# Kernel tuning notes

Measured on AMD Instinct MI355X. Metric: run time of the kernel, lower is better.

The kernel has to match this reference:

```python
import jax, jax.numpy as jnp
import numpy as np

N_USERS = 100000
N_ITEMS = 50000
N_NODES = N_USERS + N_ITEMS
LATENT = 64
NNZ = 2400000
BATCH = 2048
EPS = 1e-12  # F.normalize eps


def setup_inputs() -> dict:
    key = jax.random.key(0)
    ks = jax.random.split(key, 16)
    inp = {
        "rows": jax.random.randint(ks[0], (NNZ,), 0, N_NODES, dtype=jnp.int32),
        "cols": jax.random.randint(ks[1], (NNZ,), 0, N_NODES, dtype=jnp.int32),
        "vals": jax.random.uniform(ks[2], (NNZ,), dtype=jnp.float32),
        "x": jax.random.normal(ks[3], (N_NODES, LATENT), dtype=jnp.float32) * 0.1,
        "users": jax.random.randint(ks[12], (BATCH,), 0, N_USERS, dtype=jnp.int32),
        "items": jax.random.randint(ks[13], (BATCH,), 0, N_ITEMS, dtype=jnp.int32),
    }
    for k in range(2):
        inp[f"W_gc{k}"] = jax.random.normal(ks[4 + 4 * k], (LATENT, LATENT), dtype=jnp.float32) * 0.1
        inp[f"b_gc{k}"] = jax.random.normal(ks[5 + 4 * k], (1, LATENT), dtype=jnp.float32) * 0.1
        inp[f"W_bi{k}"] = jax.random.normal(ks[6 + 4 * k], (LATENT, LATENT), dtype=jnp.float32) * 0.1
        inp[f"b_bi{k}"] = jax.random.normal(ks[7 + 4 * k], (1, LATENT), dtype=jnp.float32) * 0.1
    return inp


def _l2_normalize(v):
    # F.normalize(p=2, dim=1): divide by max(||v||_2, eps)
    n = jnp.sqrt(jnp.sum(v * v, axis=1, keepdims=True))
    return v / jnp.maximum(n, EPS)


def reference(rows, cols, vals, x,
              W_gc0, b_gc0, W_bi0, b_bi0,
              W_gc1, b_gc1, W_bi1, b_bi1,
              users, items):
    weights = [(W_gc0, b_gc0, W_bi0, b_bi0), (W_gc1, b_gc1, W_bi1, b_bi1)]
    ego = x                      # [N, D]
    embs = [x]
    for (Wg, bg, Wb, bb) in weights:
        # sparse adj @ ego  (COO gather + segment-sum scatter)
        msgs = vals[:, None] * ego[cols]                              # [nnz, D]
        side = jax.ops.segment_sum(msgs, rows, num_segments=N_NODES)  # [N, D]
        sum_emb = side @ Wg + bg
        bi_emb = (ego * side) @ Wb + bb
        ego = _l2_normalize(jax.nn.leaky_relu(sum_emb + bi_emb, negative_slope=0.2))
        embs.append(ego)
    all_emb = jnp.concatenate(embs, axis=1)          # [N, 3*D]
    users_emb = all_emb[users]                       # [B, 3*D]
    items_emb = all_emb[N_USERS + items]             # [B, 3*D]
    gamma = jnp.sum(users_emb * items_emb, axis=1)   # [B]
    return gamma
```

## Files before the change

### kernel.cpp

```cpp
#include <hip/hip_runtime.h>

#define N_USERS_C 100000
#define N_NODES_C 150000
#define D 64
#define NB 2344
#define NSUP 74
#define CPAD 16
#define SPAD 68
#define FCAP 1536
#define S1B 256
#define FRAG 240
#define S2CAP 2560
#define BPS 16
#define FPB (S1B / BPS)

__global__ __launch_bounds__(256) void mark1_k(
    const int* __restrict__ u, const int* __restrict__ it,
    unsigned char* __restrict__ samp, unsigned char* __restrict__ need, int batch)
{
    int i = blockIdx.x * blockDim.x + threadIdx.x;
    if (i >= 2 * batch) return;
    int n = (i < batch) ? u[i] : N_USERS_C + it[i - batch];
    samp[n] = 1;
    need[n] = 1;
}

__global__ __launch_bounds__(256) void mark2_k(
    const int* __restrict__ rows, const int* __restrict__ cols,
    const unsigned char* __restrict__ samp, unsigned char* __restrict__ need, int nnz)
{
    int gtid = blockIdx.x * blockDim.x + threadIdx.x;
    int stride = gridDim.x * blockDim.x;
    for (int e = gtid; e < nnz; e += stride)
        if (samp[rows[e]]) need[cols[e]] = 1;
}

__global__ __launch_bounds__(1024) void scan1_k(
    const unsigned char* __restrict__ need, int* __restrict__ part,
    int* __restrict__ bsum, int n)
{
    __shared__ int wsum[16];
    int i = blockIdx.x * 1024 + threadIdx.x;
    int lane = threadIdx.x & 63, wid = threadIdx.x >> 6;
    int v = (i < n) ? (int)need[i] : 0;
    int incl = v;
    #pragma unroll
    for (int off = 1; off < 64; off <<= 1) {
        int t = __shfl_up(incl, off);
        if (lane >= off) incl += t;
    }
    if (lane == 63) wsum[wid] = incl;
    __syncthreads();
    int woff = 0;
    for (int w = 0; w < wid; ++w) woff += wsum[w];
    if (i < n) part[i] = woff + incl - v;
    if (threadIdx.x == 1023) bsum[blockIdx.x] = woff + incl;
}

__global__ __launch_bounds__(1024) void scan2_k(
    int* __restrict__ bsum, int nb, int* __restrict__ Mptr)
{
    __shared__ int wsum[16];
    int lane = threadIdx.x & 63, wid = threadIdx.x >> 6;
    int i = threadIdx.x;
    int v = (i < nb) ? bsum[i] : 0;
    int incl = v;
    #pragma unroll
    for (int off = 1; off < 64; off <<= 1) {
        int t = __shfl_up(incl, off);
        if (lane >= off) incl += t;
    }
    if (lane == 63) wsum[wid] = incl;
    __syncthreads();
    int woff = 0;
    for (int w = 0; w < wid; ++w) woff += wsum[w];
    if (i < nb) bsum[i] = woff + incl - v;
    if (i == nb - 1) Mptr[0] = woff + incl;
}

__global__ __launch_bounds__(256) void scan3_k(
    const int* __restrict__ bsum, int* __restrict__ idx,
    const unsigned char* __restrict__ need, int* __restrict__ list, int n)
{
    int i = blockIdx.x * blockDim.x + threadIdx.x;
    if (i >= n) return;
    int t = idx[i] + bsum[i >> 10];
    if (need[i]) { idx[i] = t; list[t] = i; }
    else idx[i] = -1;
}

__global__ __launch_bounds__(256) void initcur_k(int* __restrict__ bcur)
{
    int i = blockIdx.x * blockDim.x + threadIdx.x;
    if (i < NB) bcur[i * CPAD] = i * FCAP;
}

__global__ __launch_bounds__(512) void s1_k(
    const int* __restrict__ rows, const int* __restrict__ cols,
    const float* __restrict__ vals, const int* __restrict__ idx,
    int2* __restrict__ pairs1, int* __restrict__ scnt, int nnz)
{
    __shared__ int lcur[NSUP];
    int t = threadIdx.x;
    for (int i = t; i < NSUP; i += 512) lcur[i] = 0;
    __syncthreads();
    int b = blockIdx.x;
    int per = (nnz + S1B - 1) / S1B;
    int s = b * per;
    int e = min(nnz, s + per);
    for (int i = s + t; i < e; i += 512) {
        int ci = idx[rows[i]];
        if (ci < 0) continue;
        int sp = ci >> 11;
        int k = atomicAdd(&lcur[sp], 1);
        pairs1[(size_t)sp * (S1B * FRAG) + b * FRAG + k] =
            make_int2(((ci & 2047) << 18) | cols[i], __float_as_int(vals[i]));
    }
    __syncthreads();
    for (int i = t; i < NSUP; i += 512) scnt[i * S1B + b] = lcur[i];
}

__global__ __launch_bounds__(256) void s2_k(
    const int* __restrict__ scnt, const int2* __restrict__ pairs1,
    int* __restrict__ bcurP, int2* __restrict__ pairs)
{
    __shared__ int2 sbuf[S2CAP];
    __shared__ int fcnt[32], fcur[32], gb[32];
    int sp = blockIdx.x / BPS, part = blockIdx.x % BPS;
    int t = threadIdx.x;
    if (t < 32) { fcnt[t] = 0; fcur[t] = 0; }
    __syncthreads();
    int base = 0;
    for (int fi = 0; fi < FPB; ++fi) {
        int b = part * FPB + fi;
        int m = scnt[sp * S1B + b];
        const int2* src = &pairs1[(size_t)sp * (S1B * FRAG) + b * FRAG];
        for (int i = t; i < m; i += 256) {
            int2 p = src[i];
            sbuf[base + i] = p;
            atomicAdd(&fcnt[(p.x >> 18) >> 6], 1);
        }
        base += m;
    }
    __syncthreads();
    if (t < 32) {
        int c = fcnt[t];
        gb[t] = c ? atomicAdd(&bcurP[(sp * 32 + t) * CPAD], c) : 0;
    }
    __syncthreads();
    for (int i = t; i < base; i += 256) {
        int2 p = sbuf[i];
        int ris = p.x >> 18;
        int f = ris >> 6;
        int k = atomicAdd(&fcur[f], 1);
        pairs[gb[f] + k] = make_int2(((ris & 63) << 18) | (p.x & 0x3FFFF), p.y);
    }
}

__global__ __launch_bounds__(256) void sortb_k(
    const int* __restrict__ bcurP, int2* __restrict__ pairs,
    int* __restrict__ rp)
{
    __shared__ int2 buf[FCAP];
    __shared__ int cnt[64];
    __shared__ int cur[64];
    int b = blockIdx.x;
    int s = b * FCAP;
    int e = bcurP[b * CPAD];
    int m = e - s;
    int t = threadIdx.x;
    if (t < 64) cnt[t] = 0;
    __syncthreads();
    for (int i = t; i < m; i += 256) {
        int2 p = pairs[s + i];
        buf[i] = p;
        atomicAdd(&cnt[p.x >> 18], 1);
    }
    __syncthreads();
    if (t < 64) {
        int v = cnt[t];
        int incl = v;
        #pragma unroll
        for (int o = 1; o < 64; o <<= 1) {
            int u = __shfl_up(incl, o);
            if (t >= o) incl += u;
        }
        cur[t] = incl - v;
        rp[b * 65 + t] = s + incl - v;
        if (t == 63) rp[b * 65 + 64] = s + incl;
    }
    __syncthreads();
    for (int i = t; i < m; i += 256) {
        int2 p = buf[i];
        int dst = atomicAdd(&cur[p.x >> 18], 1);
        pairs[s + dst] = make_int2(p.x & 0x3FFFF, p.y);
    }
}

__global__ __launch_bounds__(256) void gather1_k(
    const int* __restrict__ rp, const int2* __restrict__ pairs,
    const float* __restrict__ x, float* __restrict__ side,
    const int* __restrict__ Mptr)
{
    int gtid = blockIdx.x * blockDim.x + threadIdx.x;
    int wave = gtid >> 6;
    int lane = threadIdx.x & 63;
    if (wave >= Mptr[0]) return;
    int rb = (wave >> 6) * 65 + (wave & 63);
    int s  = rp[rb];
    int ep = rp[rb + 1];

    float acc = 0.0f;
    for (int base = s; base < ep; base += 64) {
        int2 p = make_int2(0, 0);
        if (base + lane < ep) p = pairs[base + lane];
        int cnt4 = (min(ep - base, 64) + 3) & ~3;
        for (int j = 0; j < cnt4; j += 4) {
            int c0 = __shfl(p.x, j + 0);
            int c1 = __shfl(p.x, j + 1);
            int c2 = __shfl(p.x, j + 2);
            int c3 = __shfl(p.x, j + 3);
            float v0 = __int_as_float(__shfl(p.y, j + 0));
            float v1 = __int_as_float(__shfl(p.y, j + 1));
            float v2 = __int_as_float(__shfl(p.y, j + 2));
            float v3 = __int_as_float(__shfl(p.y, j + 3));
            float f0 = x[(size_t)c0 * D + lane];
            float f1 = x[(size_t)c1 * D + lane];
            float f2 = x[(size_t)c2 * D + lane];
            float f3 = x[(size_t)c3 * D + lane];
            acc = fmaf(v0, f0, acc);
            acc = fmaf(v1, f1, acc);
            acc = fmaf(v2, f2, acc);
            acc = fmaf(v3, f3, acc);
        }
    }
    side[(size_t)wave * D + lane] = acc;
}

__global__ __launch_bounds__(256) void gather2_k(
    const int* __restrict__ rp, const int2* __restrict__ pairs,
    const float* __restrict__ e1c, const int* __restrict__ idx,
    float* __restrict__ side2c, float* __restrict__ egoc,
    const int* __restrict__ u, const int* __restrict__ it, int batch)
{
    int gtid = blockIdx.x * blockDim.x + threadIdx.x;
    int wave = gtid >> 6;
    int lane = threadIdx.x & 63;
    if (wave >= 2 * batch) return;
    int n = (wave < batch) ? u[wave] : N_USERS_C + it[wave - batch];
    int cr = idx[n];
    int rb = (cr >> 6) * 65 + (cr & 63);
    int s  = rp[rb];
    int ep = rp[rb + 1];

    float acc = 0.0f;
    for (int base = s; base < ep; base += 64) {
        int2 p = make_int2(0, 0);
        if (base + lane < ep) p = pairs[base + lane];
        int cnt = min(ep - base, 64);
        for (int j = 0; j < cnt; ++j) {
            int   c = __shfl(p.x, j);
            float v = __int_as_float(__shfl(p.y, j));
            acc = fmaf(v, e1c[(size_t)idx[c] * D + lane], acc);
        }
    }
    side2c[(size_t)wave * D + lane] = acc;
    egoc[(size_t)wave * D + lane] = e1c[(size_t)cr * D + lane];
}

__global__ __launch_bounds__(256) void transform_k(
    const float* __restrict__ S, const float* __restrict__ Eb,
    const float* __restrict__ Wg, const float* __restrict__ bg,
    const float* __restrict__ Wb, const float* __restrict__ bb,
    float* __restrict__ out, const int* __restrict__ list,
    const int* __restrict__ Mptr, int nrows)
{
    __shared__ __align__(16) float sWg[D * D];
    __shared__ __align__(16) float sWb[D * D];
    __shared__ __align__(16) float sAT[D][SPAD];
    __shared__ __align__(16) float sBT[D][SPAD];

    int nr = Mptr ? Mptr[0] : nrows;
    int t  = threadIdx.x;
    int tc = t & 15;
    int tr = t >> 4;
    int r0 = blockIdx.x * 64;
    if (r0 >= nr) return;

    for (int i = t; i < D * D; i += 256) {
        sWg[i] = Wg[i];
        sWb[i] = Wb[i];
    }
    for (int itr = 0; itr < 4; ++itr) {
        int rr  = itr * 16 + (t >> 4);
        int row = r0 + rr;
        float4 sv = make_float4(0.f, 0.f, 0.f, 0.f);
        float4 ev = sv;
        if (row < nr) {
            sv = *(const float4*)&S[(size_t)row * D + tc * 4];
            int er = list ? list[row] : row;
            ev = *(const float4*)&Eb[(size_t)er * D + tc * 4];
        }
        sAT[tc * 4 + 0][rr] = sv.x;
        sAT[tc * 4 + 1][rr] = sv.y;
        sAT[tc * 4 + 2][rr] = sv.z;
        sAT[tc * 4 + 3][rr] = sv.w;
        sBT[tc * 4 + 0][rr] = sv.x * ev.x;
        sBT[tc * 4 + 1][rr] = sv.y * ev.y;
        sBT[tc * 4 + 2][rr] = sv.z * ev.z;
        sBT[tc * 4 + 3][rr] = sv.w * ev.w;
    }
    __syncthreads();

    float acc[4][4] = {};
    for (int k = 0; k < D; ++k) {
        float4 a4 = *(const float4*)&sAT[k][tr * 4];
        float4 b4 = *(const float4*)&sBT[k][tr * 4];
        float4 g4 = *(const float4*)&sWg[k * D + tc * 4];
        float4 w4 = *(const float4*)&sWb[k * D + tc * 4];
        float av[4] = {a4.x, a4.y, a4.z, a4.w};
        float bv[4] = {b4.x, b4.y, b4.z, b4.w};
        float gv[4] = {g4.x, g4.y, g4.z, g4.w};
        float wv[4] = {w4.x, w4.y, w4.z, w4.w};
        #pragma unroll
        for (int i = 0; i < 4; ++i)
            #pragma unroll
            for (int j = 0; j < 4; ++j)
                acc[i][j] = fmaf(av[i], gv[j], fmaf(bv[i], wv[j], acc[i][j]));
    }

    float4 bgv = *(const float4*)&bg[tc * 4];
    float4 bbv = *(const float4*)&bb[tc * 4];
    float bias[4] = {bgv.x + bbv.x, bgv.y + bbv.y, bgv.z + bbv.z, bgv.w + bbv.w};

    float vv[4][4];
    float ss[4] = {0.f, 0.f, 0.f, 0.f};
    #pragma unroll
    for (int i = 0; i < 4; ++i) {
        #pragma unroll
        for (int j = 0; j < 4; ++j) {
            float v = acc[i][j] + bias[j];
            v = (v > 0.0f) ? v : 0.2f * v;
            vv[i][j] = v;
            ss[i] += v * v;
        }
    }
    #pragma unroll
    for (int i = 0; i < 4; ++i) {
        #pragma unroll
        for (int off = 1; off < 16; off <<= 1)
            ss[i] += __shfl_xor(ss[i], off);
    }
    #pragma unroll
    for (int i = 0; i < 4; ++i) {
        int row = r0 + tr * 4 + i;
        if (row < nr) {
            float inv = 1.0f / fmaxf(sqrtf(ss[i]), 1e-12f);
            float4 o = make_float4(vv[i][0] * inv, vv[i][1] * inv,
                                   vv[i][2] * inv, vv[i][3] * inv);
            *(float4*)&out[(size_t)row * D + tc * 4] = o;
        }
    }
}

__global__ __launch_bounds__(256) void gamma_k(
    const float* __restrict__ x, const float* __restrict__ e1c,
    const int* __restrict__ idx, const float* __restrict__ e2c,
    const int* __restrict__ users, const int* __restrict__ items,
    float* __restrict__ gamma, int batch)
{
    int gtid = blockIdx.x * blockDim.x + threadIdx.x;
    int wave = gtid >> 6;
    int lane = threadIdx.x & 63;
    if (wave >= batch) return;
    size_t uu = (size_t)users[wave];
    size_t tt = (size_t)(N_USERS_C + items[wave]);
    float acc = x[uu * D + lane] * x[tt * D + lane]
              + e1c[(size_t)idx[uu] * D + lane] * e1c[(size_t)idx[tt] * D + lane]
              + e2c[(size_t)wave * D + lane] * e2c[(size_t)(batch + wave) * D + lane];
    #pragma unroll
    for (int off = 1; off < 64; off <<= 1) acc += __shfl_xor(acc, off);
    if (lane == 0) gamma[wave] = acc;
}

extern "C" void kernel_launch(void* const* d_in, const int* in_sizes, int n_in,
                              void* d_out, int out_size, void* d_ws, size_t ws_size,
                              hipStream_t stream) {
    const int*   rows  = (const int*)d_in[0];
    const int*   cols  = (const int*)d_in[1];
    const float* vals  = (const float*)d_in[2];
    const float* x     = (const float*)d_in[3];
    const int*   users = (const int*)d_in[4];
    const int*   items = (const int*)d_in[5];
    const float* Wg0 = (const float*)d_in[6];
    const float* bg0 = (const float*)d_in[7];
    const float* Wb0 = (const float*)d_in[8];
    const float* bb0 = (const float*)d_in[9];
    const float* Wg1 = (const float*)d_in[10];
    const float* bg1 = (const float*)d_in[11];
    const float* Wb1 = (const float*)d_in[12];
    const float* bb1 = (const float*)d_in[13];

    int nnz   = in_sizes[0];
    int batch = in_sizes[4];
    float* out = (float*)d_out;

    size_t emb = (size_t)N_NODES_C * D;
    float* A      = (float*)d_ws;
    float* Sbuf   = A + emb;
    int*   bcur   = (int*)(Sbuf + emb);
    int*   rp     = bcur + NB * CPAD;
    int*   idx    = rp + NB * 65 + 2;
    int*   list   = idx + N_NODES_C;
    int*   bsum   = list + N_NODES_C;
    int*   Mptr   = bsum + 1024;
    int*   scnt   = Mptr + 4;
    unsigned char* need = (unsigned char*)(scnt + NSUP * S1B);
    unsigned char* samp = need + N_NODES_C;
    int2*  pairs  = (int2*)(((size_t)(samp + N_NODES_C) + 15) & ~(size_t)15);

    int2*  pairs1 = (int2*)Sbuf;
    float* side2c = Sbuf;
    float* egoc   = Sbuf + (size_t)2 * 2048 * D;
    float* e2c    = egoc + (size_t)2 * 2048 * D;

    int nscan = (N_NODES_C + 1023) / 1024;

    hipMemsetAsync(need, 0, 2 * N_NODES_C, stream);
    mark1_k<<<(2 * batch + 255) / 256, 256, 0, stream>>>(users, items, samp, need, batch);
    mark2_k<<<1024, 256, 0, stream>>>(rows, cols, samp, need, nnz);
    scan1_k<<<nscan, 1024, 0, stream>>>(need, idx, bsum, N_NODES_C);
    scan2_k<<<1, 1024, 0, stream>>>(bsum, nscan, Mptr);
    scan3_k<<<(N_NODES_C + 255) / 256, 256, 0, stream>>>(bsum, idx, need, list, N_NODES_C);

    initcur_k<<<(NB + 255) / 256, 256, 0, stream>>>(bcur);
    s1_k<<<S1B, 512, 0, stream>>>(rows, cols, vals, idx, pairs1, scnt, nnz);
    s2_k<<<NSUP * BPS, 256, 0, stream>>>(scnt, pairs1, bcur, pairs);
    sortb_k<<<NB, 256, 0, stream>>>(bcur, pairs, rp);

    gather1_k<<<(N_NODES_C * 64 + 255) / 256, 256, 0, stream>>>(
        rp, pairs, x, Sbuf, Mptr);
    transform_k<<<(N_NODES_C + 63) / 64, 256, 0, stream>>>(
        Sbuf, x, Wg0, bg0, Wb0, bb0, A, list, Mptr, 0);

    gather2_k<<<(2 * batch * 64 + 255) / 256, 256, 0, stream>>>(
        rp, pairs, A, idx, side2c, egoc, users, items, batch);
    transform_k<<<(2 * batch + 63) / 64, 256, 0, stream>>>(
        side2c, egoc, Wg1, bg1, Wb1, bb1, e2c, nullptr, nullptr, 2 * batch);

    gamma_k<<<(batch * 64 + 255) / 256, 256, 0, stream>>>(
        x, A, idx, e2c, users, items, out, batch);
}
```

Before: 275.9 us.

## Fuse scan stages, bucket sort with layer-1 gather, and layer-2 gather with transform

Merges the three-pass prefix scan into two kernels by having the last finishing block scan the block sums, and folds the bucket-cursor init into the second scan pass. The per-bucket sort now keeps sorted pairs in shared memory and immediately performs the layer-1 sparse gather from LDS instead of re-reading pairs in a separate kernel. The layer-2 gather is fused with its dense transform so side and ego rows stay in shared memory. This cuts launches and global round trips. In exchange it doubles LDS use in the sort kernel, which may lower occupancy, and serialises gathers within each wave.

```diff
diff --git a/kernel.cpp b/kernel.cpp
--- a/kernel.cpp
+++ b/kernel.cpp
@@ -16,9 +16,11 @@
 
 __global__ __launch_bounds__(256) void mark1_k(
     const int* __restrict__ u, const int* __restrict__ it,
-    unsigned char* __restrict__ samp, unsigned char* __restrict__ need, int batch)
+    unsigned char* __restrict__ samp, unsigned char* __restrict__ need,
+    int* __restrict__ tcnt, int batch)
 {
     int i = blockIdx.x * blockDim.x + threadIdx.x;
+    if (i == 0) *tcnt = 0;
     if (i >= 2 * batch) return;
     int n = (i < batch) ? u[i] : N_USERS_C + it[i - batch];
     samp[n] = 1;
@@ -35,11 +37,13 @@
         if (samp[rows[e]]) need[cols[e]] = 1;
 }
 
-__global__ __launch_bounds__(1024) void scan1_k(
+__global__ __launch_bounds__(1024) void scanA_k(
     const unsigned char* __restrict__ need, int* __restrict__ part,
-    int* __restrict__ bsum, int n)
+    int* __restrict__ bsum, int* __restrict__ tcnt, int* __restrict__ Mptr,
+    int n, int nblocks)
 {
     __shared__ int wsum[16];
+    __shared__ int isLast;
     int i = blockIdx.x * 1024 + threadIdx.x;
     int lane = threadIdx.x & 63, wid = threadIdx.x >> 6;
     int v = (i < n) ? (int)need[i] : 0;
@@ -55,44 +59,40 @@
     for (int w = 0; w < wid; ++w) woff += wsum[w];
     if (i < n) part[i] = woff + incl - v;
     if (threadIdx.x == 1023) bsum[blockIdx.x] = woff + incl;
-}
-
-__global__ __launch_bounds__(1024) void scan2_k(
-    int* __restrict__ bsum, int nb, int* __restrict__ Mptr)
-{
-    __shared__ int wsum[16];
-    int lane = threadIdx.x & 63, wid = threadIdx.x >> 6;
-    int i = threadIdx.x;
-    int v = (i < nb) ? bsum[i] : 0;
-    int incl = v;
+
+    __threadfence();
+    if (threadIdx.x == 0) isLast = (atomicAdd(tcnt, 1) == nblocks - 1);
+    __syncthreads();
+    if (!isLast) return;
+    __threadfence();
+    int j = threadIdx.x;
+    int bv = (j < nblocks) ? atomicAdd(&bsum[j], 0) : 0;
+    int bincl = bv;
     #pragma unroll
     for (int off = 1; off < 64; off <<= 1) {
-        int t = __shfl_up(incl, off);
-        if (lane >= off) incl += t;
-    }
-    if (lane == 63) wsum[wid] = incl;
-    __syncthreads();
-    int woff = 0;
-    for (int w = 0; w < wid; ++w) woff += wsum[w];
-    if (i < nb) bsum[i] = woff + incl - v;
-    if (i == nb - 1) Mptr[0] = woff + incl;
-}
-
-__global__ __launch_bounds__(256) void scan3_k(
+        int t = __shfl_up(bincl, off);
+        if (lane >= off) bincl += t;
+    }
+    __syncthreads();
+    if (lane == 63) wsum[wid] = bincl;
+    __syncthreads();
+    int woff2 = 0;
+    for (int w = 0; w < wid; ++w) woff2 += wsum[w];
+    if (j < nblocks) bsum[j] = woff2 + bincl - bv;
+    if (j == nblocks - 1) Mptr[0] = woff2 + bincl;
+}
+
+__global__ __launch_bounds__(256) void scanB_k(
     const int* __restrict__ bsum, int* __restrict__ idx,
-    const unsigned char* __restrict__ need, int* __restrict__ list, int n)
+    const unsigned char* __restrict__ need, int* __restrict__ list,
+    int* __restrict__ bcur, int n)
 {
     int i = blockIdx.x * blockDim.x + threadIdx.x;
+    if (i < NB) bcur[i * CPAD] = i * FCAP;
     if (i >= n) return;
     int t = idx[i] + bsum[i >> 10];
     if (need[i]) { idx[i] = t; list[t] = i; }
     else idx[i] = -1;
-}
-
-__global__ __launch_bounds__(256) void initcur_k(int* __restrict__ bcur)
-{
-    int i = blockIdx.x * blockDim.x + threadIdx.x;
-    if (i < NB) bcur[i * CPAD] = i * FCAP;
 }
 
 __global__ __launch_bounds__(512) void s1_k(
@@ -157,18 +157,19 @@
     }
 }
 
-__global__ __launch_bounds__(256) void sortb_k(
+__global__ __launch_bounds__(256) void gs1_k(
     const int* __restrict__ bcurP, int2* __restrict__ pairs,
-    int* __restrict__ rp)
+    int* __restrict__ rp, const float* __restrict__ x,
+    float* __restrict__ side, const int* __restrict__ Mptr)
 {
     __shared__ int2 buf[FCAP];
-    __shared__ int cnt[64];
-    __shared__ int cur[64];
+    __shared__ int2 obuf[FCAP];
+    __shared__ int cnt[64], cur[64], rs[65];
     int b = blockIdx.x;
+    if (b * 64 >= Mptr[0]) return;
     int s = b * FCAP;
-    int e = bcurP[b * CPAD];
-    int m = e - s;
-    int t = threadIdx.x;
+    int m = bcurP[b * CPAD] - s;
+    int t = threadIdx.x, lane = t & 63, wid = t >> 6;
     if (t < 64) cnt[t] = 0;
     __syncthreads();
     for (int i = t; i < m; i += 256) {
@@ -178,94 +179,48 @@
     }
     __syncthreads();
     if (t < 64) {
-        int v = cnt[t];
-        int incl = v;
+        int v = cnt[t], incl = v;
         #pragma unroll
         for (int o = 1; o < 64; o <<= 1) {
             int u = __shfl_up(incl, o);
             if (t >= o) incl += u;
         }
+        rs[t] = incl - v;
         cur[t] = incl - v;
         rp[b * 65 + t] = s + incl - v;
-        if (t == 63) rp[b * 65 + 64] = s + incl;
+        if (t == 63) { rs[64] = incl; rp[b * 65 + 64] = s + incl; }
     }
     __syncthreads();
     for (int i = t; i < m; i += 256) {
         int2 p = buf[i];
         int dst = atomicAdd(&cur[p.x >> 18], 1);
-        pairs[s + dst] = make_int2(p.x & 0x3FFFF, p.y);
-    }
-}
-
-__global__ __launch_bounds__(256) void gather1_k(
-    const int* __restrict__ rp, const int2* __restrict__ pairs,
-    const float* __restrict__ x, float* __restrict__ side,
-    const int* __restrict__ Mptr)
-{
-    int gtid = blockIdx.x * blockDim.x + threadIdx.x;
-    int wave = gtid >> 6;
-    int lane = threadIdx.x & 63;
-    if (wave >= Mptr[0]) return;
-    int rb = (wave >> 6) * 65 + (wave & 63);
-    int s  = rp[rb];
-    int ep = rp[rb + 1];
-
-    float acc = 0.0f;
-    for (int base = s; base < ep; base += 64) {
-        int2 p = make_int2(0, 0);
-        if (base + lane < ep) p = pairs[base + lane];
-        int cnt4 = (min(ep - base, 64) + 3) & ~3;
-        for (int j = 0; j < cnt4; j += 4) {
-            int c0 = __shfl(p.x, j + 0);
-            int c1 = __shfl(p.x, j + 1);
-            int c2 = __shfl(p.x, j + 2);
-            int c3 = __shfl(p.x, j + 3);
-            float v0 = __int_as_float(__shfl(p.y, j + 0));
-            float v1 = __int_as_float(__shfl(p.y, j + 1));
-            float v2 = __int_as_float(__shfl(p.y, j + 2));
-            float v3 = __int_as_float(__shfl(p.y, j + 3));
-            float f0 = x[(size_t)c0 * D + lane];
-            float f1 = x[(size_t)c1 * D + lane];
-            float f2 = x[(size_t)c2 * D + lane];
-            float f3 = x[(size_t)c3 * D + lane];
-            acc = fmaf(v0, f0, acc);
-            acc = fmaf(v1, f1, acc);
-            acc = fmaf(v2, f2, acc);
-            acc = fmaf(v3, f3, acc);
-        }
-    }
-    side[(size_t)wave * D + lane] = acc;
-}
-
-__global__ __launch_bounds__(256) void gather2_k(
-    const int* __restrict__ rp, const int2* __restrict__ pairs,
-    const float* __restrict__ e1c, const int* __restrict__ idx,
-    float* __restrict__ side2c, float* __restrict__ egoc,
-    const int* __restrict__ u, const int* __restrict__ it, int batch)
-{
-    int gtid = blockIdx.x * blockDim.x + threadIdx.x;
-    int wave = gtid >> 6;
-    int lane = threadIdx.x & 63;
-    if (wave >= 2 * batch) return;
-    int n = (wave < batch) ? u[wave] : N_USERS_C + it[wave - batch];
-    int cr = idx[n];
-    int rb = (cr >> 6) * 65 + (cr & 63);
-    int s  = rp[rb];
-    int ep = rp[rb + 1];
-
-    float acc = 0.0f;
-    for (int base = s; base < ep; base += 64) {
-        int2 p = make_int2(0, 0);
-        if (base + lane < ep) p = pairs[base + lane];
-        int cnt = min(ep - base, 64);
-        for (int j = 0; j < cnt; ++j) {
-            int   c = __shfl(p.x, j);
-            float v = __int_as_float(__shfl(p.y, j));
-            acc = fmaf(v, e1c[(size_t)idx[c] * D + lane], acc);
-        }
-    }
-    side2c[(size_t)wave * D + lane] = acc;
-    egoc[(size_t)wave * D + lane] = e1c[(size_t)cr * D + lane];
+        obuf[dst] = make_int2(p.x & 0x3FFFF, p.y);
+    }
+    __syncthreads();
+    for (int i = t; i < m; i += 256)
+        pairs[s + i] = obuf[i];
+
+    for (int j = wid * 16; j < wid * 16 + 16; ++j) {
+        int k  = rs[j];
+        int re = rs[j + 1];
+        float acc = 0.0f;
+        for (; k + 8 <= re; k += 8) {
+            float vv[8], ff[8];
+            #pragma unroll
+            for (int q = 0; q < 8; ++q) {
+                int2 p = obuf[k + q];
+                vv[q] = __int_as_float(p.y);
+                ff[q] = x[(size_t)p.x * D + lane];
+            }
+            #pragma unroll
+            for (int q = 0; q < 8; ++q) acc = fmaf(vv[q], ff[q], acc);
+        }
+        for (; k < re; ++k) {
+            int2 p = obuf[k];
+            acc = fmaf(__int_as_float(p.y), x[(size_t)p.x * D + lane], acc);
+        }
+        side[((size_t)b * 64 + j) * D + lane] = acc;
+    }
 }
 
 __global__ __launch_bounds__(256) void transform_k(
@@ -273,14 +228,14 @@
     const float* __restrict__ Wg, const float* __restrict__ bg,
     const float* __restrict__ Wb, const float* __restrict__ bb,
     float* __restrict__ out, const int* __restrict__ list,
-    const int* __restrict__ Mptr, int nrows)
+    const int* __restrict__ Mptr)
 {
     __shared__ __align__(16) float sWg[D * D];
     __shared__ __align__(16) float sWb[D * D];
     __shared__ __align__(16) float sAT[D][SPAD];
     __shared__ __align__(16) float sBT[D][SPAD];
 
-    int nr = Mptr ? Mptr[0] : nrows;
+    int nr = Mptr[0];
     int t  = threadIdx.x;
     int tc = t & 15;
     int tr = t >> 4;
@@ -298,8 +253,7 @@
         float4 ev = sv;
         if (row < nr) {
             sv = *(const float4*)&S[(size_t)row * D + tc * 4];
-            int er = list ? list[row] : row;
-            ev = *(const float4*)&Eb[(size_t)er * D + tc * 4];
+            ev = *(const float4*)&Eb[(size_t)list[row] * D + tc * 4];
         }
         sAT[tc * 4 + 0][rr] = sv.x;
         sAT[tc * 4 + 1][rr] = sv.y;
@@ -359,6 +313,101 @@
             float4 o = make_float4(vv[i][0] * inv, vv[i][1] * inv,
                                    vv[i][2] * inv, vv[i][3] * inv);
             *(float4*)&out[(size_t)row * D + tc * 4] = o;
+        }
+    }
+}
+
+__global__ __launch_bounds__(256) void gt2_k(
+    const int* __restrict__ rp, const int2* __restrict__ pairs,
+    const float* __restrict__ e1c, const int* __restrict__ idx,
+    const float* __restrict__ Wg, const float* __restrict__ bg,
+    const float* __restrict__ Wb, const float* __restrict__ bb,
+    float* __restrict__ e2c, const int* __restrict__ u,
+    const int* __restrict__ it, int batch)
+{
+    __shared__ __align__(16) float sWg[D * D];
+    __shared__ __align__(16) float sWb[D * D];
+    __shared__ __align__(16) float sAT[D][SPAD];
+    __shared__ __align__(16) float sBT[D][SPAD];
+
+    int t = threadIdx.x, lane = t & 63, wid = t >> 6;
+    int r0 = blockIdx.x * 64;
+    int nr = 2 * batch;
+    for (int i = t; i < D * D; i += 256) { sWg[i] = Wg[i]; sWb[i] = Wb[i]; }
+
+    for (int jj = 0; jj < 16; ++jj) {
+        int j = wid * 16 + jj;
+        int r = r0 + j;
+        float acc = 0.0f, ev = 0.0f;
+        if (r < nr) {
+            int n = (r < batch) ? u[r] : N_USERS_C + it[r - batch];
+            int cr = idx[n];
+            int rb = (cr >> 6) * 65 + (cr & 63);
+            int s = rp[rb], ep = rp[rb + 1];
+            for (int base = s; base < ep; base += 64) {
+                int2 p = make_int2(0, 0);
+                if (base + lane < ep) p = pairs[base + lane];
+                int cc = min(ep - base, 64);
+                for (int q = 0; q < cc; ++q) {
+                    int   c = __shfl(p.x, q);
+                    float v = __int_as_float(__shfl(p.y, q));
+                    acc = fmaf(v, e1c[(size_t)idx[c] * D + lane], acc);
+                }
+            }
+            ev = e1c[(size_t)cr * D + lane];
+        }
+        sAT[lane][j] = acc;
+        sBT[lane][j] = acc * ev;
+    }
+    __syncthreads();
+
+    int tc = t & 15;
+    int tr = t >> 4;
+    float acc[4][4] = {};
+    for (int k = 0; k < D; ++k) {
+        float4 a4 = *(const float4*)&sAT[k][tr * 4];
+        float4 b4 = *(const float4*)&sBT[k][tr * 4];
+        float4 g4 = *(const float4*)&sWg[k * D + tc * 4];
+        float4 w4 = *(const float4*)&sWb[k * D + tc * 4];
+        float av[4] = {a4.x, a4.y, a4.z, a4.w};
+        float bv[4] = {b4.x, b4.y, b4.z, b4.w};
+        float gv[4] = {g4.x, g4.y, g4.z, g4.w};
+        float wv[4] = {w4.x, w4.y, w4.z, w4.w};
+        #pragma unroll
+        for (int i = 0; i < 4; ++i)
+            #pragma unroll
+            for (int j = 0; j < 4; ++j)
+                acc[i][j] = fmaf(av[i], gv[j], fmaf(bv[i], wv[j], acc[i][j]));
+    }
+    float4 bgv = *(const float4*)&bg[tc * 4];
+    float4 bbv = *(const float4*)&bb[tc * 4];
+    float bias[4] = {bgv.x + bbv.x, bgv.y + bbv.y, bgv.z + bbv.z, bgv.w + bbv.w};
+    float vv[4][4];
+    float ss[4] = {0.f, 0.f, 0.f, 0.f};
+    #pragma unroll
+    for (int i = 0; i < 4; ++i) {
+        #pragma unroll
+        for (int j = 0; j < 4; ++j) {
+            float v = acc[i][j] + bias[j];
+            v = (v > 0.0f) ? v : 0.2f * v;
+            vv[i][j] = v;
+            ss[i] += v * v;
+        }
+    }
+    #pragma unroll
+    for (int i = 0; i < 4; ++i) {
+        #pragma unroll
+        for (int off = 1; off < 16; off <<= 1)
+            ss[i] += __shfl_xor(ss[i], off);
+    }
+    #pragma unroll
+    for (int i = 0; i < 4; ++i) {
+        int row = r0 + tr * 4 + i;
+        if (row < nr) {
+            float inv = 1.0f / fmaxf(sqrtf(ss[i]), 1e-12f);
+            float4 o = make_float4(vv[i][0] * inv, vv[i][1] * inv,
+                                   vv[i][2] * inv, vv[i][3] * inv);
+            *(float4*)&e2c[(size_t)row * D + tc * 4] = o;
         }
     }
 }
@@ -420,33 +469,25 @@
     int2*  pairs  = (int2*)(((size_t)(samp + N_NODES_C) + 15) & ~(size_t)15);
 
     int2*  pairs1 = (int2*)Sbuf;
-    float* side2c = Sbuf;
-    float* egoc   = Sbuf + (size_t)2 * 2048 * D;
-    float* e2c    = egoc + (size_t)2 * 2048 * D;
+    float* e2c    = Sbuf;
 
     int nscan = (N_NODES_C + 1023) / 1024;
 
     hipMemsetAsync(need, 0, 2 * N_NODES_C, stream);
-    mark1_k<<<(2 * batch + 255) / 256, 256, 0, stream>>>(users, items, samp, need, batch);
+    mark1_k<<<(2 * batch + 255) / 256, 256, 0, stream>>>(users, items, samp, need, Mptr + 1, batch);
     mark2_k<<<1024, 256, 0, stream>>>(rows, cols, samp, need, nnz);
-    scan1_k<<<nscan, 1024, 0, stream>>>(need, idx, bsum, N_NODES_C);
-    scan2_k<<<1, 1024, 0, stream>>>(bsum, nscan, Mptr);
-    scan3_k<<<(N_NODES_C + 255) / 256, 256, 0, stream>>>(bsum, idx, need, list, N_NODES_C);
-
-    initcur_k<<<(NB + 255) / 256, 256, 0, stream>>>(bcur);
+    scanA_k<<<nscan, 1024, 0, stream>>>(need, idx, bsum, Mptr + 1, Mptr, N_NODES_C, nscan);
+    scanB_k<<<(N_NODES_C + 255) / 256, 256, 0, stream>>>(bsum, idx, need, list, bcur, N_NODES_C);
+
     s1_k<<<S1B, 512, 0, stream>>>(rows, cols, vals, idx, pairs1, scnt, nnz);
     s2_k<<<NSUP * BPS, 256, 0, stream>>>(scnt, pairs1, bcur, pairs);
-    sortb_k<<<NB, 256, 0, stream>>>(bcur, pairs, rp);
-
-    gather1_k<<<(N_NODES_C * 64 + 255) / 256, 256, 0, stream>>>(
-        rp, pairs, x, Sbuf, Mptr);
+
+    gs1_k<<<NB, 256, 0, stream>>>(bcur, pairs, rp, x, Sbuf, Mptr);
     transform_k<<<(N_NODES_C + 63) / 64, 256, 0, stream>>>(
-        Sbuf, x, Wg0, bg0, Wb0, bb0, A, list, Mptr, 0);
-
-    gather2_k<<<(2 * batch * 64 + 255) / 256, 256, 0, stream>>>(
-        rp, pairs, A, idx, side2c, egoc, users, items, batch);
-    transform_k<<<(2 * batch + 63) / 64, 256, 0, stream>>>(
-        side2c, egoc, Wg1, bg1, Wb1, bb1, e2c, nullptr, nullptr, 2 * batch);
+        Sbuf, x, Wg0, bg0, Wb0, bb0, A, list, Mptr);
+
+    gt2_k<<<(2 * batch + 63) / 64, 256, 0, stream>>>(
+        rp, pairs, A, idx, Wg1, bg1, Wb1, bb1, e2c, users, items, batch);
 
     gamma_k<<<(batch * 64 + 255) / 256, 256, 0, stream>>>(
         x, A, idx, e2c, users, items, out, batch);
```

Result: slower. 467.2 us (+69.3%).

## Merge scan kernels via last-block pattern and unroll gather by eight

Applied to the files above, without the earlier changes.

Fuses the three-pass scan into two kernels. The last block to finish, found with an atomic ticket counter, performs the block-sum scan, and the bcur initialization is folded into the scatter pass. This removes two kernel launches and their serialization gaps. Separately, the gather1 inner loop is unrolled from 4 to 8 independent row loads to expose more memory-level parallelism, at the cost of more registers and extra padded iterations for short rows.

```diff
diff --git a/kernel.cpp b/kernel.cpp
--- a/kernel.cpp
+++ b/kernel.cpp
@@ -16,9 +16,11 @@
 
 __global__ __launch_bounds__(256) void mark1_k(
     const int* __restrict__ u, const int* __restrict__ it,
-    unsigned char* __restrict__ samp, unsigned char* __restrict__ need, int batch)
+    unsigned char* __restrict__ samp, unsigned char* __restrict__ need,
+    int* __restrict__ tcnt, int batch)
 {
     int i = blockIdx.x * blockDim.x + threadIdx.x;
+    if (i == 0) *tcnt = 0;
     if (i >= 2 * batch) return;
     int n = (i < batch) ? u[i] : N_USERS_C + it[i - batch];
     samp[n] = 1;
@@ -35,11 +37,13 @@
         if (samp[rows[e]]) need[cols[e]] = 1;
 }
 
-__global__ __launch_bounds__(1024) void scan1_k(
+__global__ __launch_bounds__(1024) void scanA_k(
     const unsigned char* __restrict__ need, int* __restrict__ part,
-    int* __restrict__ bsum, int n)
+    int* __restrict__ bsum, int* __restrict__ tcnt, int* __restrict__ Mptr,
+    int n, int nblocks)
 {
     __shared__ int wsum[16];
+    __shared__ int isLast;
     int i = blockIdx.x * 1024 + threadIdx.x;
     int lane = threadIdx.x & 63, wid = threadIdx.x >> 6;
     int v = (i < n) ? (int)need[i] : 0;
@@ -55,44 +59,40 @@
     for (int w = 0; w < wid; ++w) woff += wsum[w];
     if (i < n) part[i] = woff + incl - v;
     if (threadIdx.x == 1023) bsum[blockIdx.x] = woff + incl;
-}
-
-__global__ __launch_bounds__(1024) void scan2_k(
-    int* __restrict__ bsum, int nb, int* __restrict__ Mptr)
-{
-    __shared__ int wsum[16];
-    int lane = threadIdx.x & 63, wid = threadIdx.x >> 6;
-    int i = threadIdx.x;
-    int v = (i < nb) ? bsum[i] : 0;
-    int incl = v;
+
+    __threadfence();
+    if (threadIdx.x == 0) isLast = (atomicAdd(tcnt, 1) == nblocks - 1);
+    __syncthreads();
+    if (!isLast) return;
+    __threadfence();
+    int j = threadIdx.x;
+    int bv = (j < nblocks) ? atomicAdd(&bsum[j], 0) : 0;
+    int bincl = bv;
     #pragma unroll
     for (int off = 1; off < 64; off <<= 1) {
-        int t = __shfl_up(incl, off);
-        if (lane >= off) incl += t;
-    }
-    if (lane == 63) wsum[wid] = incl;
-    __syncthreads();
-    int woff = 0;
-    for (int w = 0; w < wid; ++w) woff += wsum[w];
-    if (i < nb) bsum[i] = woff + incl - v;
-    if (i == nb - 1) Mptr[0] = woff + incl;
-}
-
-__global__ __launch_bounds__(256) void scan3_k(
+        int t = __shfl_up(bincl, off);
+        if (lane >= off) bincl += t;
+    }
+    __syncthreads();
+    if (lane == 63) wsum[wid] = bincl;
+    __syncthreads();
+    int woff2 = 0;
+    for (int w = 0; w < wid; ++w) woff2 += wsum[w];
+    if (j < nblocks) bsum[j] = woff2 + bincl - bv;
+    if (j == nblocks - 1) Mptr[0] = woff2 + bincl;
+}
+
+__global__ __launch_bounds__(256) void scanB_k(
     const int* __restrict__ bsum, int* __restrict__ idx,
-    const unsigned char* __restrict__ need, int* __restrict__ list, int n)
+    const unsigned char* __restrict__ need, int* __restrict__ list,
+    int* __restrict__ bcur, int n)
 {
     int i = blockIdx.x * blockDim.x + threadIdx.x;
+    if (i < NB) bcur[i * CPAD] = i * FCAP;
     if (i >= n) return;
     int t = idx[i] + bsum[i >> 10];
     if (need[i]) { idx[i] = t; list[t] = i; }
     else idx[i] = -1;
-}
-
-__global__ __launch_bounds__(256) void initcur_k(int* __restrict__ bcur)
-{
-    int i = blockIdx.x * blockDim.x + threadIdx.x;
-    if (i < NB) bcur[i * CPAD] = i * FCAP;
 }
 
 __global__ __launch_bounds__(512) void s1_k(
@@ -214,24 +214,20 @@
     for (int base = s; base < ep; base += 64) {
         int2 p = make_int2(0, 0);
         if (base + lane < ep) p = pairs[base + lane];
-        int cnt4 = (min(ep - base, 64) + 3) & ~3;
-        for (int j = 0; j < cnt4; j += 4) {
-            int c0 = __shfl(p.x, j + 0);
-            int c1 = __shfl(p.x, j + 1);
-            int c2 = __shfl(p.x, j + 2);
-            int c3 = __shfl(p.x, j + 3);
-            float v0 = __int_as_float(__shfl(p.y, j + 0));
-            float v1 = __int_as_float(__shfl(p.y, j + 1));
-            float v2 = __int_as_float(__shfl(p.y, j + 2));
-            float v3 = __int_as_float(__shfl(p.y, j + 3));
-            float f0 = x[(size_t)c0 * D + lane];
-            float f1 = x[(size_t)c1 * D + lane];
-            float f2 = x[(size_t)c2 * D + lane];
-            float f3 = x[(size_t)c3 * D + lane];
-            acc = fmaf(v0, f0, acc);
-            acc = fmaf(v1, f1, acc);
-            acc = fmaf(v2, f2, acc);
-            acc = fmaf(v3, f3, acc);
+        int cnt8 = (min(ep - base, 64) + 7) & ~7;
+        for (int j = 0; j < cnt8; j += 8) {
+            int cc[8]; float vv[8], ff[8];
+            #pragma unroll
+            for (int q = 0; q < 8; ++q) {
+                cc[q] = __shfl(p.x, j + q);
+                vv[q] = __int_as_float(__shfl(p.y, j + q));
+            }
+            #pragma unroll
+            for (int q = 0; q < 8; ++q)
+                ff[q] = x[(size_t)cc[q] * D + lane];
+            #pragma unroll
+            for (int q = 0; q < 8; ++q)
+                acc = fmaf(vv[q], ff[q], acc);
         }
     }
     side[(size_t)wave * D + lane] = acc;
@@ -427,13 +423,11 @@
     int nscan = (N_NODES_C + 1023) / 1024;
 
     hipMemsetAsync(need, 0, 2 * N_NODES_C, stream);
-    mark1_k<<<(2 * batch + 255) / 256, 256, 0, stream>>>(users, items, samp, need, batch);
+    mark1_k<<<(2 * batch + 255) / 256, 256, 0, stream>>>(users, items, samp, need, Mptr + 1, batch);
     mark2_k<<<1024, 256, 0, stream>>>(rows, cols, samp, need, nnz);
-    scan1_k<<<nscan, 1024, 0, stream>>>(need, idx, bsum, N_NODES_C);
-    scan2_k<<<1, 1024, 0, stream>>>(bsum, nscan, Mptr);
-    scan3_k<<<(N_NODES_C + 255) / 256, 256, 0, stream>>>(bsum, idx, need, list, N_NODES_C);
-
-    initcur_k<<<(NB + 255) / 256, 256, 0, stream>>>(bcur);
+    scanA_k<<<nscan, 1024, 0, stream>>>(need, idx, bsum, Mptr + 1, Mptr, N_NODES_C, nscan);
+    scanB_k<<<(N_NODES_C + 255) / 256, 256, 0, stream>>>(bsum, idx, need, list, bcur, N_NODES_C);
+
     s1_k<<<S1B, 512, 0, stream>>>(rows, cols, vals, idx, pairs1, scnt, nnz);
     s2_k<<<NSUP * BPS, 256, 0, stream>>>(scnt, pairs1, bcur, pairs);
     sortb_k<<<NB, 256, 0, stream>>>(bcur, pairs, rp);
```

Result: slower. 319.6 us (+15.8%).
